# Kernel tuning notes

Measured on AMD Instinct MI355X. Metric: run time of the kernel, lower is better.

Reference implementation:

```python
import jax, jax.numpy as jnp
import numpy as np

B, NQ, NKV, D = 2, 2048, 4096, 1024
H, DH = 16, 64            # qk_channels = v_channels = 1024 -> 16 heads x 64
HID = 2 * int(4.0 * D)    # GEGLU produces 8192 -> split into 2x4096
EPS = 1e-6


def layernorm(x, scale, bias):
    mu = jnp.mean(x, axis=-1, keepdims=True)
    var = jnp.mean(jnp.square(x - mu), axis=-1, keepdims=True)
    return (x - mu) * jax.lax.rsqrt(var + EPS) * scale + bias


def setup_inputs() -> dict:
    key = jax.random.key(0)
    ks = jax.random.split(key, 12)
    s = 0.02
    return {
        "inputs_q": jax.random.normal(ks[0], (B, NQ, D), jnp.float32),
        "inputs_kv": jax.random.normal(ks[1], (B, NKV, D), jnp.float32),
        "ln_q_scale": jnp.ones((D,), jnp.float32),
        "ln_q_bias": jnp.zeros((D,), jnp.float32),
        "ln_kv_scale": jnp.ones((D,), jnp.float32),
        "ln_kv_bias": jnp.zeros((D,), jnp.float32),
        "Wq": s * jax.random.normal(ks[2], (D, H, DH), jnp.float32),
        "bq": jnp.zeros((H, DH), jnp.float32),
        "Wk": s * jax.random.normal(ks[3], (D, H, DH), jnp.float32),
        "bk": jnp.zeros((H, DH), jnp.float32),
        "Wv": s * jax.random.normal(ks[4], (D, H, DH), jnp.float32),
        "bv": jnp.zeros((H, DH), jnp.float32),
        "Wo": s * jax.random.normal(ks[5], (H, DH, D), jnp.float32),
        "bo": jnp.zeros((D,), jnp.float32),
        "ln2_scale": jnp.ones((D,), jnp.float32),
        "ln2_bias": jnp.zeros((D,), jnp.float32),
        "W1": s * jax.random.normal(ks[6], (D, HID), jnp.float32),
        "b1": jnp.zeros((HID,), jnp.float32),
        "W2": s * jax.random.normal(ks[7], (HID // 2, D), jnp.float32),
        "b2": jnp.zeros((D,), jnp.float32),
    }


def reference(inputs_q, inputs_kv, ln_q_scale, ln_q_bias, ln_kv_scale, ln_kv_bias,
              Wq, bq, Wk, bk, Wv, bv, Wo, bo, ln2_scale, ln2_bias, W1, b1, W2, b2):
    ln_q = layernorm(inputs_q, ln_q_scale, ln_q_bias)
    ln_kv = layernorm(inputs_kv, ln_kv_scale, ln_kv_bias)
    # multi-head projections: DenseGeneral to (H, DH)
    q = jnp.einsum('bqd,dhe->bqhe', ln_q, Wq) + bq
    k = jnp.einsum('bkd,dhe->bkhe', ln_kv, Wk) + bk
    v = jnp.einsum('bkd,dhe->bkhe', ln_kv, Wv) + bv
    # scaled dot-product attention (full score matrix, as in source)
    attn = jnp.einsum('bqhd,bkhd->bhqk', q, k) / np.sqrt(DH).astype(np.float32)
    attn = jax.nn.softmax(attn, axis=-1)
    o = jnp.einsum('bhqk,bkhd->bqhd', attn, v)
    # output projection contracting (H, DH)
    x = jnp.einsum('bqhd,hdo->bqo', o, Wo) + bo
    x = x + inputs_q  # query residual
    # GEGLU MLP
    h = layernorm(x, ln2_scale, ln2_bias)
    h = jnp.dot(h, W1) + b1
    a, g = jnp.split(h, 2, axis=-1)
    h = a * jax.nn.gelu(g)  # approximate (tanh) gelu, flax default
    y = jnp.dot(h, W2) + b2
    return x + y
```

## Files before the change

### kernel.cpp

```cpp
#include <hip/hip_runtime.h>

typedef unsigned short u16;
typedef unsigned int u32;
typedef float f32x4 __attribute__((ext_vector_type(4)));
typedef float f32x16 __attribute__((ext_vector_type(16)));
typedef __bf16 bf16x8 __attribute__((ext_vector_type(8)));
typedef short s16x8 __attribute__((ext_vector_type(8)));
typedef short s16x4 __attribute__((ext_vector_type(4)));
typedef u32 u32x4 __attribute__((ext_vector_type(4)));

#define MFMA16(a, b, c) __builtin_amdgcn_mfma_f32_16x16x32_bf16((a), (b), (c), 0, 0, 0)
#define MFMA32(a, b, c) __builtin_amdgcn_mfma_f32_32x32x16_bf16((a), (b), (c), 0, 0, 0)

typedef const __attribute__((address_space(1))) void* gas1_t;
typedef __attribute__((address_space(3))) void* las3_t;
#define GLDS16(g, l) __builtin_amdgcn_global_load_lds((gas1_t)(g), (las3_t)(l), 16, 0, 0)

static __device__ __forceinline__ u16 f2bf(float f) {
  u32 u = __builtin_bit_cast(u32, f);
  u += 0x7FFFu + ((u >> 16) & 1u);
  return (u16)(u >> 16);
}
static __device__ __forceinline__ u32 cvtpk(float lo, float hi) {
  u32 r;
  asm("v_cvt_pk_bf16_f32 %0, %1, %2" : "=v"(r) : "v"(lo), "v"(hi));
  return r;
}
static __device__ __forceinline__ float gelu_t(float g) {
  float u = 0.7978845608f * (g + 0.044715f * g * g * g);
  float e = __expf(2.0f * u);
  float t = 1.0f - 2.0f / (e + 1.0f);
  return 0.5f * g * (1.0f + t);
}

__global__ __launch_bounds__(256) void prep_weights(const float* __restrict__ Wq,
                                                    const float* __restrict__ Wk,
                                                    const float* __restrict__ Wv,
                                                    const float* __restrict__ Wo,
                                                    const float* __restrict__ W1,
                                                    const float* __restrict__ W2,
                                                    u16* __restrict__ wqt,
                                                    u16* __restrict__ wkvt,
                                                    u16* __restrict__ wot,
                                                    u16* __restrict__ w1i,
                                                    u16* __restrict__ w2t, float qsc) {
  __shared__ u16 t[64][72];
  const int id = blockIdx.x;
  const int tid = threadIdx.x;
  auto tileT = [&](const float* in, u16* out, int K, int N, int k0, int n0, float scale) {
#pragma unroll
    for (int i = 0; i < 16; ++i) {
      int idx = tid + i * 256;
      int r = idx >> 6, c = idx & 63;
      t[r][c] = f2bf(in[(size_t)(k0 + r) * N + n0 + c] * scale);
    }
    __syncthreads();
#pragma unroll
    for (int i = 0; i < 16; ++i) {
      int idx = tid + i * 256;
      int r = idx >> 6, c = idx & 63;
      out[(size_t)(n0 + r) * K + k0 + c] = t[c][r];
    }
  };
  if (id < 256) {
    tileT(Wq, wqt, 1024, 1024, (id & 15) * 64, (id >> 4) * 64, qsc);
  } else if (id < 512) {
    int i2 = id - 256;
    tileT(Wk, wkvt, 1024, 1024, (i2 & 15) * 64, (i2 >> 4) * 64, 1.0f);
  } else if (id < 768) {
    int i2 = id - 512;
    tileT(Wv, wkvt + 1024 * 1024, 1024, 1024, (i2 & 15) * 64, (i2 >> 4) * 64, 1.0f);
  } else if (id < 1024) {
    int i2 = id - 768;
    tileT(Wo, wot, 1024, 1024, (i2 & 15) * 64, (i2 >> 4) * 64, 1.0f);
  } else if (id < 3072) {
    int i2 = id - 1024;
    int k0 = (i2 & 15) * 64, n0 = (i2 >> 4) * 64;
#pragma unroll
    for (int i = 0; i < 16; ++i) {
      int idx = tid + i * 256;
      int r = idx >> 6, c = idx & 63;
      int np = n0 + c;
      int orig = ((np >> 5) << 4) + (np & 15) + (((np >> 4) & 1) << 12);
      t[r][c] = f2bf(W1[(size_t)(k0 + r) * 8192 + orig]);
    }
    __syncthreads();
#pragma unroll
    for (int i = 0; i < 16; ++i) {
      int idx = tid + i * 256;
      int r = idx >> 6, c = idx & 63;
      w1i[(size_t)(n0 + r) * 1024 + k0 + c] = t[c][r];
    }
  } else {
    int i3 = id - 3072;
    tileT(W2, w2t, 4096, 1024, (i3 & 63) * 64, (i3 >> 6) * 64, 1.0f);
  }
}

__global__ __launch_bounds__(256) void ln_fused(const float* __restrict__ xq,
                                                const float* __restrict__ xkv,
                                                const float* __restrict__ scq,
                                                const float* __restrict__ biq,
                                                const float* __restrict__ sckv,
                                                const float* __restrict__ bikv,
                                                u16* __restrict__ outq,
                                                u16* __restrict__ outkv) {
  const int id = blockIdx.x;
  const bool isq = id < 4096;
  const int row = isq ? id : id - 4096;
  const float* x = isq ? xq : xkv;
  const float* sc = isq ? scq : sckv;
  const float* bi = isq ? biq : bikv;
  u16* out = isq ? outq : outkv;
  int tid = threadIdx.x;
  float4 v = ((const float4*)(x + (size_t)row * 1024))[tid];
  float s = v.x + v.y + v.z + v.w;
  float s2 = v.x * v.x + v.y * v.y + v.z * v.z + v.w * v.w;
  for (int m = 1; m < 64; m <<= 1) {
    s += __shfl_xor(s, m);
    s2 += __shfl_xor(s2, m);
  }
  __shared__ float rs[4], rs2[4];
  int wave = tid >> 6, lane = tid & 63;
  if (lane == 0) { rs[wave] = s; rs2[wave] = s2; }
  __syncthreads();
  s = rs[0] + rs[1] + rs[2] + rs[3];
  s2 = rs2[0] + rs2[1] + rs2[2] + rs2[3];
  float mu = s * (1.0f / 1024.0f);
  float var = s2 * (1.0f / 1024.0f) - mu * mu;
  float inv = rsqrtf(var + 1e-6f);
  float4 scv = ((const float4*)sc)[tid];
  float4 biv = ((const float4*)bi)[tid];
  s16x4 o;
  o[0] = (short)f2bf((v.x - mu) * inv * scv.x + biv.x);
  o[1] = (short)f2bf((v.y - mu) * inv * scv.y + biv.y);
  o[2] = (short)f2bf((v.z - mu) * inv * scv.z + biv.z);
  o[3] = (short)f2bf((v.w - mu) * inv * scv.w + biv.w);
  *(s16x4*)(out + (size_t)row * 1024 + tid * 4) = o;
}

template <int MODE>
__global__ __launch_bounds__(256) void gemm_nt(const u16* __restrict__ A,
                                               const u16* __restrict__ Bt,
                                               const float* __restrict__ bias,
                                               const float* __restrict__ resid,
                                               void* __restrict__ Cout,
                                               int M, int N, int K, float bias_scale) {
  __shared__ u16 As[128 * 64];
  __shared__ u16 Bs[128 * 64];
  const int nbx = gridDim.x;
  const int nwg = nbx * gridDim.y;
  const int wg0 = blockIdx.y * nbx + blockIdx.x;
  const int wg = (nwg & 7) ? wg0 : (wg0 & 7) * (nwg >> 3) + (wg0 >> 3);
  const int m0 = (wg % nbx) * 128, n0 = (wg / nbx) * 128;
  const int tid = threadIdx.x;
  const int lane = tid & 63, wave = tid >> 6;
  const int wm = (wave >> 1) * 64, wn = (wave & 1) * 64;
  const int lr = lane & 15, hi4 = lane >> 4;
  f32x4 acc[4][4] = {};
  for (int k0 = 0; k0 < K; k0 += 64) {
#pragma unroll
    for (int i = 0; i < 4; ++i) {
      int s = i * 256 + tid;
      int r = s >> 3, slot = s & 7;
      int gslot = slot ^ (r & 7);
      int ldst = (i * 256 + wave * 64) * 8;
      GLDS16(A + (size_t)(m0 + r) * K + k0 + gslot * 8, &As[ldst]);
      GLDS16(Bt + (size_t)(n0 + r) * K + k0 + gslot * 8, &Bs[ldst]);
    }
    __syncthreads();
#pragma unroll
    for (int ks = 0; ks < 2; ++ks) {
      const int sl = ((ks * 4 + hi4) ^ (lr & 7)) * 8;
      bf16x8 af[4], bfr[4];
#pragma unroll
      for (int t = 0; t < 4; ++t) {
        af[t] = __builtin_bit_cast(bf16x8, *(const s16x8*)&As[(wm + t * 16 + lr) * 64 + sl]);
        bfr[t] = __builtin_bit_cast(bf16x8, *(const s16x8*)&Bs[(wn + t * 16 + lr) * 64 + sl]);
      }
#pragma unroll
      for (int mt = 0; mt < 4; ++mt)
#pragma unroll
        for (int nt = 0; nt < 4; ++nt)
          acc[mt][nt] = MFMA16(af[mt], bfr[nt], acc[mt][nt]);
    }
    __syncthreads();
  }
#pragma unroll
  for (int mt = 0; mt < 4; ++mt) {
#pragma unroll
    for (int nt = 0; nt < 4; ++nt) {
      const int ncol = n0 + wn + nt * 16 + lr;
      const float bv = bias[ncol] * bias_scale;
      const int mbase = m0 + wm + mt * 16 + hi4 * 4;
#pragma unroll
      for (int r = 0; r < 4; ++r) {
        const int m = mbase + r;
        const float val = acc[mt][nt][r] + bv;
        if constexpr (MODE == 0) {
          ((u16*)Cout)[(size_t)m * N + ncol] = f2bf(val);
        } else {
          ((float*)Cout)[(size_t)m * N + ncol] = val + resid[(size_t)m * N + ncol];
        }
      }
    }
  }
}

template <int MODE>
__global__ __launch_bounds__(512, 2) void gemm256(const u16* __restrict__ A,
                                                  const u16* __restrict__ Bt,
                                                  const float* __restrict__ bias,
                                                  const float* __restrict__ bias2,
                                                  u16* __restrict__ Cout,
                                                  u16* __restrict__ Vout,
                                                  int M, int N, int K, int nmajor) {
  __shared__ __align__(16) u16 sA[2][2][256 * 32];
  __shared__ __align__(16) u16 sB[2][2][256 * 32];
  const int nbx = M >> 8, nby = N >> 8;
  const int nblk = nbx * nby;
  const int cpx = nblk >> 3;
  const int wg0 = blockIdx.x;
  const int wg = (wg0 & 7) * cpx + (wg0 >> 3);
  int mi, ni;
  if (nmajor) { ni = wg % nby; mi = wg / nby; } else { mi = wg % nbx; ni = wg / nbx; }
  const int m0 = mi << 8, n0 = ni << 8;
  const int tid = threadIdx.x;
  const int lane = tid & 63, wave = tid >> 6;
  const int wr = wave >> 2, wc = wave & 3;
  const int lr = lane & 15, hi4 = lane >> 4;
  const int rdoct = (hi4 ^ ((lr >> 1) & 3)) * 8;
  const int NT = K >> 6;

  auto stageA = [&](int t, int kh) {
#pragma unroll
    for (int i = 0; i < 2; ++i) {
      int idx = i * 512 + tid;
      int r = idx >> 2, go = (idx & 3) ^ ((r >> 1) & 3);
      GLDS16(A + (size_t)(m0 + r) * K + t * 64 + kh * 32 + go * 8,
             &sA[t & 1][kh][(i * 512 + wave * 64) * 8]);
    }
  };
  auto stageB = [&](int t, int kh) {
#pragma unroll
    for (int i = 0; i < 2; ++i) {
      int idx = i * 512 + tid;
      int r = idx >> 2, go = (idx & 3) ^ ((r >> 1) & 3);
      GLDS16(Bt + (size_t)(n0 + r) * K + t * 64 + kh * 32 + go * 8,
             &sB[t & 1][kh][(i * 512 + wave * 64) * 8]);
    }
  };

  f32x4 acc[8][4] = {};
  bf16x8 af[4], bf[4];

  stageA(0, 0); stageB(0, 0); stageA(0, 1); stageB(0, 1);
  asm volatile("s_waitcnt vmcnt(4)" ::: "memory");
  __builtin_amdgcn_s_barrier();
  __builtin_amdgcn_sched_barrier(0);

  for (int t = 0; t < NT; ++t) {
    const int buf = t & 1;
    const bool pre = (t + 1 < NT);
#pragma unroll
    for (int kh = 0; kh < 2; ++kh) {
#pragma unroll
      for (int nt = 0; nt < 4; ++nt)
        bf[nt] = __builtin_bit_cast(bf16x8,
            *(const s16x8*)&sB[buf][kh][(wc * 64 + nt * 16 + lr) * 32 + rdoct]);
#pragma unroll
      for (int mf = 0; mf < 4; ++mf)
        af[mf] = __builtin_bit_cast(bf16x8,
            *(const s16x8*)&sA[buf][kh][(wr * 128 + mf * 16 + lr) * 32 + rdoct]);
      if (pre) stageA(t + 1, kh);
      __builtin_amdgcn_s_barrier();
      asm volatile("s_waitcnt lgkmcnt(0)" ::: "memory");
      __builtin_amdgcn_sched_barrier(0);
      __builtin_amdgcn_s_setprio(1);
#pragma unroll
      for (int mf = 0; mf < 4; ++mf)
#pragma unroll
        for (int nt = 0; nt < 4; ++nt)
          acc[mf][nt] = MFMA16(af[mf], bf[nt], acc[mf][nt]);
      __builtin_amdgcn_s_setprio(0);
      __builtin_amdgcn_s_barrier();
      __builtin_amdgcn_sched_barrier(0);
#pragma unroll
      for (int mf = 0; mf < 4; ++mf)
        af[mf] = __builtin_bit_cast(bf16x8,
            *(const s16x8*)&sA[buf][kh][(wr * 128 + (4 + mf) * 16 + lr) * 32 + rdoct]);
      if (pre) stageB(t + 1, kh);
      __builtin_amdgcn_s_barrier();
      asm volatile("s_waitcnt lgkmcnt(0)" ::: "memory");
      __builtin_amdgcn_sched_barrier(0);
      __builtin_amdgcn_s_setprio(1);
#pragma unroll
      for (int mf = 0; mf < 4; ++mf)
#pragma unroll
        for (int nt = 0; nt < 4; ++nt)
          acc[4 + mf][nt] = MFMA16(af[mf], bf[nt], acc[4 + mf][nt]);
      __builtin_amdgcn_s_setprio(0);
      if (pre)
        asm volatile("s_waitcnt vmcnt(4)" ::: "memory");
      else
        asm volatile("s_waitcnt vmcnt(0)" ::: "memory");
      __builtin_amdgcn_s_barrier();
      __builtin_amdgcn_sched_barrier(0);
    }
  }

  if constexpr (MODE == 0) {
#pragma unroll
    for (int mf = 0; mf < 8; ++mf) {
#pragma unroll
      for (int nt = 0; nt < 4; ++nt) {
        const int ncol = n0 + wc * 64 + nt * 16 + lr;
        const int mbase = m0 + wr * 128 + mf * 16 + hi4 * 4;
        const bool isk = ncol < 1024;
        const int vc = isk ? ncol : ncol - 1024;
        const float bv = isk ? bias[ncol] : bias2[vc];
#pragma unroll
        for (int r = 0; r < 4; ++r) {
          const int m = mbase + r;
          const float val = acc[mf][nt][r] + bv;
          if (isk) {
            Cout[(size_t)m * 1024 + ncol] = f2bf(val);
          } else {
            size_t vidx = ((size_t)((m >> 12) * 1024 + vc) << 12) | (size_t)(m & 4095);
            Vout[vidx] = f2bf(val);
          }
        }
      }
    }
  } else {
#pragma unroll
    for (int mf = 0; mf < 8; ++mf) {
      const int mbase = m0 + wr * 128 + mf * 16 + hi4 * 4;
#pragma unroll
      for (int p = 0; p < 2; ++p) {
        const int oc = (((n0 + wc * 64 + p * 32) >> 5) << 4) + lr;
        const float ba = bias[oc];
        const float bg = bias[oc + 4096];
#pragma unroll
        for (int r = 0; r < 4; ++r) {
          const int m = mbase + r;
          float a = acc[mf][2 * p][r] + ba;
          float g = acc[mf][2 * p + 1][r] + bg;
          Cout[(size_t)m * 4096 + oc] = f2bf(a * gelu_t(g));
        }
      }
    }
  }
}

__global__ __launch_bounds__(128, 3) void flash_attn(const u16* __restrict__ Qg,
                                                     const u16* __restrict__ Kg,
                                                     const u16* __restrict__ Vt,
                                                     u16* __restrict__ Og) {
  __shared__ u16 Ks[2][64 * 64];
  __shared__ u16 Vs[2][64 * 64];
  const int id = blockIdx.x;
  const int bh = (id & 7) * 4 + ((id >> 3) & 3);
  const int qb = id >> 5;
  const int b = bh >> 4, h = bh & 15;
  const int q0 = qb * 64;
  const int tid = threadIdx.x;
  const int lane = tid & 63, wave = tid >> 6;
  const int lq = lane & 31, hi = lane >> 5;
  const u16* Kbase = Kg + (size_t)(b * 4096) * 1024 + h * 64;
  const u16* Vbase = Vt + (size_t)((b * 16 + h) * 64) * 4096;
  bf16x8 qf[4];
  const size_t qrow = (size_t)(b * 2048 + q0 + wave * 32 + lq);
#pragma unroll
  for (int dc = 0; dc < 4; ++dc)
    qf[dc] = __builtin_bit_cast(bf16x8, *(const s16x8*)&Qg[qrow * 1024 + h * 64 + dc * 16 + hi * 8]);

  const u32x4 onesw = {0x3F803F80u, 0x3F803F80u, 0x3F803F80u, 0x3F803F80u};
  const bf16x8 ones = __builtin_bit_cast(bf16x8, onesw);
  f32x16 oacc0 = {}, oacc1 = {}, accl = {};

  auto stage = [&](int buf, int tile) {
    const int kv0 = tile * 64;
#pragma unroll
    for (int i = 0; i < 4; ++i) {
      int s = i * 128 + tid;
      int r = s >> 3;
      int inb = ((s & 7) * 16) ^ ((r & 7) << 4);
      GLDS16(Kbase + (size_t)(kv0 + r) * 1024 + (inb >> 1), &Ks[buf][s * 8]);
    }
#pragma unroll
    for (int i = 0; i < 4; ++i) {
      int s = i * 128 + tid;
      int r = s >> 3;
      int inb = ((s & 7) * 16) ^ ((r & 7) << 4);
      GLDS16(Vbase + (size_t)r * 4096 + kv0 + (inb >> 1), &Vs[buf][s * 8]);
    }
  };

  stage(0, 0);
  __syncthreads();
  int cur = 0;
  for (int t = 0; t < 64; ++t) {
    if (t < 63) stage(cur ^ 1, t + 1);
    f32x16 sA = {}, sB = {};
    __builtin_amdgcn_s_setprio(1);
#pragma unroll
    for (int dc = 0; dc < 4; ++dc) {
      int row = lq;
      int inb = (dc * 32 + hi * 16) ^ ((row & 7) << 4);
      bf16x8 kf = __builtin_bit_cast(bf16x8, *(const s16x8*)&Ks[cur][row * 64 + (inb >> 1)]);
      sA = MFMA32(kf, qf[dc], sA);
    }
#pragma unroll
    for (int dc = 0; dc < 4; ++dc) {
      int row = 32 + lq;
      int inb = (dc * 32 + hi * 16) ^ ((row & 7) << 4);
      bf16x8 kf = __builtin_bit_cast(bf16x8, *(const s16x8*)&Ks[cur][row * 64 + (inb >> 1)]);
      sB = MFMA32(kf, qf[dc], sB);
    }
    __builtin_amdgcn_s_setprio(0);
    bf16x8 vf0[4];
#pragma unroll
    for (int c = 0; c < 2; ++c) {
#pragma unroll
      for (int half = 0; half < 2; ++half) {
        int row = half * 32 + lq;
        int inb = (c * 32 + hi * 16) ^ ((row & 7) << 4);
        vf0[c * 2 + half] = __builtin_bit_cast(bf16x8, *(const s16x8*)&Vs[cur][row * 64 + (inb >> 1)]);
      }
    }
#pragma unroll
    for (int i = 0; i < 16; ++i) sA[i] = __builtin_amdgcn_exp2f(sA[i]);
#pragma unroll
    for (int i = 0; i < 16; ++i) sB[i] = __builtin_amdgcn_exp2f(sB[i]);
    u32 wa[8], wb[8];
#pragma unroll
    for (int i = 0; i < 8; ++i) wa[i] = cvtpk(sA[2 * i], sA[2 * i + 1]);
#pragma unroll
    for (int i = 0; i < 8; ++i) wb[i] = cvtpk(sB[2 * i], sB[2 * i + 1]);
    u32 a0 = wa[0], c0 = wa[2];
    asm("v_permlane32_swap_b32 %0, %1" : "+v"(a0), "+v"(c0));
    u32 a1 = wa[1], c1 = wa[3];
    asm("v_permlane32_swap_b32 %0, %1" : "+v"(a1), "+v"(c1));
    u32 a2 = wa[4], c2 = wa[6];
    asm("v_permlane32_swap_b32 %0, %1" : "+v"(a2), "+v"(c2));
    u32 a3 = wa[5], c3 = wa[7];
    asm("v_permlane32_swap_b32 %0, %1" : "+v"(a3), "+v"(c3));
    u32 e0 = wb[0], g0 = wb[2];
    asm("v_permlane32_swap_b32 %0, %1" : "+v"(e0), "+v"(g0));
    u32 e1 = wb[1], g1 = wb[3];
    asm("v_permlane32_swap_b32 %0, %1" : "+v"(e1), "+v"(g1));
    u32 e2 = wb[4], g2 = wb[6];
    asm("v_permlane32_swap_b32 %0, %1" : "+v"(e2), "+v"(g2));
    u32 e3 = wb[5], g3 = wb[7];
    asm("v_permlane32_swap_b32 %0, %1" : "+v"(e3), "+v"(g3));
    u32x4 t00 = {a0, a1, c0, c1};
    u32x4 t01 = {a2, a3, c2, c3};
    u32x4 t10 = {e0, e1, g0, g1};
    u32x4 t11 = {e2, e3, g2, g3};
    bf16x8 pf[4] = {__builtin_bit_cast(bf16x8, t00), __builtin_bit_cast(bf16x8, t01),
                    __builtin_bit_cast(bf16x8, t10), __builtin_bit_cast(bf16x8, t11)};
    __builtin_amdgcn_s_setprio(1);
#pragma unroll
    for (int c = 0; c < 2; ++c) {
      oacc0 = MFMA32(vf0[c * 2 + 0], pf[c], oacc0);
      oacc1 = MFMA32(vf0[c * 2 + 1], pf[c], oacc1);
      accl = MFMA32(ones, pf[c], accl);
    }
#pragma unroll
    for (int c = 0; c < 2; ++c) {
      {
        int row = lq;
        int inb = (64 + c * 32 + hi * 16) ^ ((row & 7) << 4);
        bf16x8 vf = __builtin_bit_cast(bf16x8, *(const s16x8*)&Vs[cur][row * 64 + (inb >> 1)]);
        oacc0 = MFMA32(vf, pf[2 + c], oacc0);
      }
      {
        int row = 32 + lq;
        int inb = (64 + c * 32 + hi * 16) ^ ((row & 7) << 4);
        bf16x8 vf = __builtin_bit_cast(bf16x8, *(const s16x8*)&Vs[cur][row * 64 + (inb >> 1)]);
        oacc1 = MFMA32(vf, pf[2 + c], oacc1);
      }
      accl = MFMA32(ones, pf[2 + c], accl);
    }
    __builtin_amdgcn_s_setprio(0);
    __syncthreads();
    cur ^= 1;
  }
  float rinv = 1.0f / accl[0];
  u16* obase = Og + qrow * 1024 + h * 64;
#pragma unroll
  for (int rp = 0; rp < 8; ++rp) {
    int r0 = rp * 2;
    int d0 = (r0 & 3) + 8 * (r0 >> 2) + 4 * hi;
    *(u32*)&obase[d0] = cvtpk(oacc0[r0] * rinv, oacc0[r0 + 1] * rinv);
    *(u32*)&obase[32 + d0] = cvtpk(oacc1[r0] * rinv, oacc1[r0 + 1] * rinv);
  }
}

extern "C" void kernel_launch(void* const* d_in, const int* in_sizes, int n_in,
                              void* d_out, int out_size, void* d_ws, size_t ws_size,
                              hipStream_t stream) {
  (void)in_sizes; (void)n_in; (void)out_size; (void)ws_size;
  const float* inputs_q = (const float*)d_in[0];
  const float* inputs_kv = (const float*)d_in[1];
  const float* ln_q_scale = (const float*)d_in[2];
  const float* ln_q_bias = (const float*)d_in[3];
  const float* ln_kv_scale = (const float*)d_in[4];
  const float* ln_kv_bias = (const float*)d_in[5];
  const float* Wq = (const float*)d_in[6];
  const float* bq = (const float*)d_in[7];
  const float* Wk = (const float*)d_in[8];
  const float* bk = (const float*)d_in[9];
  const float* Wv = (const float*)d_in[10];
  const float* bv = (const float*)d_in[11];
  const float* Wo = (const float*)d_in[12];
  const float* bo = (const float*)d_in[13];
  const float* ln2_scale = (const float*)d_in[14];
  const float* ln2_bias = (const float*)d_in[15];
  const float* W1 = (const float*)d_in[16];
  const float* b1 = (const float*)d_in[17];
  const float* W2 = (const float*)d_in[18];
  const float* b2 = (const float*)d_in[19];
  float* out = (float*)d_out;
  char* ws = (char*)d_ws;
  const size_t MB = 1ull << 20;
  u16* lnq = (u16*)(ws + 0);
  u16* lnkv = (u16*)(ws + 8 * MB);
  u16* Qb = (u16*)(ws + 24 * MB);
  u16* Kb = (u16*)(ws + 32 * MB);
  u16* Vtb = (u16*)(ws + 48 * MB);
  u16* Ob = (u16*)(ws + 64 * MB);
  float* xbuf = (float*)(ws + 72 * MB);
  u16* ln2b = (u16*)(ws + 88 * MB);
  u16* gg = (u16*)(ws + 96 * MB);
  u16* wqt = (u16*)(ws + 128 * MB);
  u16* wkvt = (u16*)(ws + 130 * MB);
  u16* wot = (u16*)(ws + 134 * MB);
  u16* w1i = (u16*)(ws + 136 * MB);
  u16* w2t = (u16*)(ws + 152 * MB);

  const float QSC = 0.125f * 1.44269504088896f;
  dim3 blk(256);
  prep_weights<<<dim3(4096), blk, 0, stream>>>(Wq, Wk, Wv, Wo, W1, W2, wqt, wkvt, wot, w1i, w2t, QSC);
  ln_fused<<<dim3(12288), blk, 0, stream>>>(inputs_q, inputs_kv, ln_q_scale, ln_q_bias,
                                            ln_kv_scale, ln_kv_bias, lnq, lnkv);
  gemm_nt<0><<<dim3(32, 8), blk, 0, stream>>>(lnq, wqt, bq, nullptr, Qb, 4096, 1024, 1024, QSC);
  gemm256<0><<<dim3(256), dim3(512), 0, stream>>>(lnkv, wkvt, bk, bv, Kb, Vtb, 8192, 2048, 1024, 1);
  flash_attn<<<dim3(1024), dim3(128), 0, stream>>>(Qb, Kb, Vtb, Ob);
  gemm_nt<2><<<dim3(32, 8), blk, 0, stream>>>(Ob, wot, bo, inputs_q, xbuf, 4096, 1024, 1024, 1.0f);
  ln_fused<<<dim3(4096), blk, 0, stream>>>(xbuf, xbuf, ln2_scale, ln2_bias, ln2_scale, ln2_bias,
                                           ln2b, ln2b);
  gemm256<1><<<dim3(512), dim3(512), 0, stream>>>(ln2b, w1i, b1, nullptr, gg, nullptr, 4096, 8192, 1024, 0);
  gemm_nt<2><<<dim3(32, 8), blk, 0, stream>>>(gg, w2t, b2, xbuf, out, 4096, 1024, 4096, 1.0f);
}
```

Measured before the change: 408.0 us.

## Restructure flash attention: 256-row query tiles, triple-buffered KV, VALU row sums

```diff
diff --git a/kernel.cpp b/kernel.cpp
--- a/kernel.cpp
+++ b/kernel.cpp
@@ -353,148 +353,171 @@
   }
 }
 
-__global__ __launch_bounds__(128, 3) void flash_attn(const u16* __restrict__ Qg,
+__global__ __launch_bounds__(256, 1) void flash_attn(const u16* __restrict__ Qg,
                                                      const u16* __restrict__ Kg,
                                                      const u16* __restrict__ Vt,
                                                      u16* __restrict__ Og) {
-  __shared__ u16 Ks[2][64 * 64];
-  __shared__ u16 Vs[2][64 * 64];
+  __shared__ u16 Ks[3][64 * 64];
+  __shared__ u16 Vs[3][64 * 64];
   const int id = blockIdx.x;
-  const int bh = (id & 7) * 4 + ((id >> 3) & 3);
+  const int rr = id & 31;
+  const int bh = (rr & 7) * 4 + (rr >> 3);
   const int qb = id >> 5;
   const int b = bh >> 4, h = bh & 15;
-  const int q0 = qb * 64;
+  const int q0 = qb * 256;
   const int tid = threadIdx.x;
   const int lane = tid & 63, wave = tid >> 6;
   const int lq = lane & 31, hi = lane >> 5;
   const u16* Kbase = Kg + (size_t)(b * 4096) * 1024 + h * 64;
   const u16* Vbase = Vt + (size_t)((b * 16 + h) * 64) * 4096;
-  bf16x8 qf[4];
-  const size_t qrow = (size_t)(b * 2048 + q0 + wave * 32 + lq);
-#pragma unroll
-  for (int dc = 0; dc < 4; ++dc)
-    qf[dc] = __builtin_bit_cast(bf16x8, *(const s16x8*)&Qg[qrow * 1024 + h * 64 + dc * 16 + hi * 8]);
-
-  const u32x4 onesw = {0x3F803F80u, 0x3F803F80u, 0x3F803F80u, 0x3F803F80u};
-  const bf16x8 ones = __builtin_bit_cast(bf16x8, onesw);
-  f32x16 oacc0 = {}, oacc1 = {}, accl = {};
+  bf16x8 qf0[4], qf1[4];
+  const size_t qrow0 = (size_t)(b * 2048 + q0 + wave * 64 + lq);
+  const size_t qrow1 = qrow0 + 32;
+#pragma unroll
+  for (int dc = 0; dc < 4; ++dc) {
+    qf0[dc] = __builtin_bit_cast(bf16x8, *(const s16x8*)&Qg[qrow0 * 1024 + h * 64 + dc * 16 + hi * 8]);
+    qf1[dc] = __builtin_bit_cast(bf16x8, *(const s16x8*)&Qg[qrow1 * 1024 + h * 64 + dc * 16 + hi * 8]);
+  }
+  f32x16 oacc00 = {}, oacc01 = {}, oacc10 = {}, oacc11 = {};
+  float l0 = 0.0f, l1 = 0.0f;
 
   auto stage = [&](int buf, int tile) {
     const int kv0 = tile * 64;
 #pragma unroll
-    for (int i = 0; i < 4; ++i) {
-      int s = i * 128 + tid;
+    for (int i = 0; i < 2; ++i) {
+      int s = i * 256 + tid;
       int r = s >> 3;
       int inb = ((s & 7) * 16) ^ ((r & 7) << 4);
-      GLDS16(Kbase + (size_t)(kv0 + r) * 1024 + (inb >> 1), &Ks[buf][s * 8]);
-    }
-#pragma unroll
-    for (int i = 0; i < 4; ++i) {
-      int s = i * 128 + tid;
+      GLDS16(Kbase + (size_t)(kv0 + r) * 1024 + (inb >> 1), &Ks[buf][(i * 256 + wave * 64) * 8]);
+    }
+#pragma unroll
+    for (int i = 0; i < 2; ++i) {
+      int s = i * 256 + tid;
       int r = s >> 3;
       int inb = ((s & 7) * 16) ^ ((r & 7) << 4);
-      GLDS16(Vbase + (size_t)r * 4096 + kv0 + (inb >> 1), &Vs[buf][s * 8]);
+      GLDS16(Vbase + (size_t)r * 4096 + kv0 + (inb >> 1), &Vs[buf][(i * 256 + wave * 64) * 8]);
     }
   };
 
+  auto softpack = [&](f32x16 sA, f32x16 sB, bf16x8* pf, float& lrun) {
+#pragma unroll
+    for (int i = 0; i < 16; ++i) sA[i] = __builtin_amdgcn_exp2f(sA[i]);
+#pragma unroll
+    for (int i = 0; i < 16; ++i) sB[i] = __builtin_amdgcn_exp2f(sB[i]);
+    float a0 = (sA[0] + sA[1]) + (sA[2] + sA[3]);
+    float a1 = (sA[4] + sA[5]) + (sA[6] + sA[7]);
+    float a2 = (sA[8] + sA[9]) + (sA[10] + sA[11]);
+    float a3 = (sA[12] + sA[13]) + (sA[14] + sA[15]);
+    float b0 = (sB[0] + sB[1]) + (sB[2] + sB[3]);
+    float b1 = (sB[4] + sB[5]) + (sB[6] + sB[7]);
+    float b2 = (sB[8] + sB[9]) + (sB[10] + sB[11]);
+    float b3 = (sB[12] + sB[13]) + (sB[14] + sB[15]);
+    float ts = ((a0 + a1) + (a2 + a3)) + ((b0 + b1) + (b2 + b3));
+    ts += __shfl_xor(ts, 32);
+    lrun += ts;
+    u32 wa[8], wb[8];
+#pragma unroll
+    for (int i = 0; i < 8; ++i) wa[i] = cvtpk(sA[2 * i], sA[2 * i + 1]);
+#pragma unroll
+    for (int i = 0; i < 8; ++i) wb[i] = cvtpk(sB[2 * i], sB[2 * i + 1]);
+    u32 x0 = wa[0], y0 = wa[2];
+    asm("v_permlane32_swap_b32 %0, %1" : "+v"(x0), "+v"(y0));
+    u32 x1 = wa[1], y1 = wa[3];
+    asm("v_permlane32_swap_b32 %0, %1" : "+v"(x1), "+v"(y1));
+    u32 x2 = wa[4], y2 = wa[6];
+    asm("v_permlane32_swap_b32 %0, %1" : "+v"(x2), "+v"(y2));
+    u32 x3 = wa[5], y3 = wa[7];
+    asm("v_permlane32_swap_b32 %0, %1" : "+v"(x3), "+v"(y3));
+    u32 z0 = wb[0], u0 = wb[2];
+    asm("v_permlane32_swap_b32 %0, %1" : "+v"(z0), "+v"(u0));
+    u32 z1 = wb[1], u1 = wb[3];
+    asm("v_permlane32_swap_b32 %0, %1" : "+v"(z1), "+v"(u1));
+    u32 z2 = wb[4], u2 = wb[6];
+    asm("v_permlane32_swap_b32 %0, %1" : "+v"(z2), "+v"(u2));
+    u32 z3 = wb[5], u3 = wb[7];
+    asm("v_permlane32_swap_b32 %0, %1" : "+v"(z3), "+v"(u3));
+    u32x4 t00 = {x0, x1, y0, y1};
+    u32x4 t01 = {x2, x3, y2, y3};
+    u32x4 t10 = {z0, z1, u0, u1};
+    u32x4 t11 = {z2, z3, u2, u3};
+    pf[0] = __builtin_bit_cast(bf16x8, t00);
+    pf[1] = __builtin_bit_cast(bf16x8, t01);
+    pf[2] = __builtin_bit_cast(bf16x8, t10);
+    pf[3] = __builtin_bit_cast(bf16x8, t11);
+  };
+
   stage(0, 0);
-  __syncthreads();
-  int cur = 0;
+  stage(1, 1);
+  asm volatile("s_waitcnt vmcnt(4)" ::: "memory");
+  __builtin_amdgcn_s_barrier();
+  __builtin_amdgcn_sched_barrier(0);
+
   for (int t = 0; t < 64; ++t) {
-    if (t < 63) stage(cur ^ 1, t + 1);
+    const int buf = t % 3;
+    if (t + 2 < 64) stage((t + 2) % 3, t + 2);
+    bf16x8 kf[8];
+#pragma unroll
+    for (int st = 0; st < 2; ++st)
+#pragma unroll
+      for (int dc = 0; dc < 4; ++dc) {
+        int row = st * 32 + lq;
+        int inb = (dc * 32 + hi * 16) ^ ((row & 7) << 4);
+        kf[st * 4 + dc] = __builtin_bit_cast(bf16x8, *(const s16x8*)&Ks[buf][row * 64 + (inb >> 1)]);
+      }
     f32x16 sA = {}, sB = {};
     __builtin_amdgcn_s_setprio(1);
 #pragma unroll
-    for (int dc = 0; dc < 4; ++dc) {
-      int row = lq;
-      int inb = (dc * 32 + hi * 16) ^ ((row & 7) << 4);
-      bf16x8 kf = __builtin_bit_cast(bf16x8, *(const s16x8*)&Ks[cur][row * 64 + (inb >> 1)]);
-      sA = MFMA32(kf, qf[dc], sA);
-    }
-#pragma unroll
-    for (int dc = 0; dc < 4; ++dc) {
-      int row = 32 + lq;
-      int inb = (dc * 32 + hi * 16) ^ ((row & 7) << 4);
-      bf16x8 kf = __builtin_bit_cast(bf16x8, *(const s16x8*)&Ks[cur][row * 64 + (inb >> 1)]);
-      sB = MFMA32(kf, qf[dc], sB);
-    }
+    for (int dc = 0; dc < 4; ++dc) sA = MFMA32(kf[dc], qf0[dc], sA);
+#pragma unroll
+    for (int dc = 0; dc < 4; ++dc) sB = MFMA32(kf[4 + dc], qf0[dc], sB);
     __builtin_amdgcn_s_setprio(0);
-    bf16x8 vf0[4];
-#pragma unroll
-    for (int c = 0; c < 2; ++c) {
-#pragma unroll
-      for (int half = 0; half < 2; ++half) {
-        int row = half * 32 + lq;
-        int inb = (c * 32 + hi * 16) ^ ((row & 7) << 4);
-        vf0[c * 2 + half] = __builtin_bit_cast(bf16x8, *(const s16x8*)&Vs[cur][row * 64 + (inb >> 1)]);
+    bf16x8 pf0[4];
+    softpack(sA, sB, pf0, l0);
+    f32x16 tA = {}, tB = {};
+    __builtin_amdgcn_s_setprio(1);
+#pragma unroll
+    for (int dc = 0; dc < 4; ++dc) tA = MFMA32(kf[dc], qf1[dc], tA);
+#pragma unroll
+    for (int dc = 0; dc < 4; ++dc) tB = MFMA32(kf[4 + dc], qf1[dc], tB);
+    __builtin_amdgcn_s_setprio(0);
+    bf16x8 pf1[4];
+    softpack(tA, tB, pf1, l1);
+    __builtin_amdgcn_s_setprio(1);
+#pragma unroll
+    for (int st = 0; st < 2; ++st)
+#pragma unroll
+      for (int c = 0; c < 2; ++c) {
+        const int pi = st * 2 + c;
+        int rowa = lq;
+        int inba = (st * 64 + c * 32 + hi * 16) ^ ((rowa & 7) << 4);
+        bf16x8 vfa = __builtin_bit_cast(bf16x8, *(const s16x8*)&Vs[buf][rowa * 64 + (inba >> 1)]);
+        int rowb = 32 + lq;
+        int inbb = (st * 64 + c * 32 + hi * 16) ^ ((rowb & 7) << 4);
+        bf16x8 vfb = __builtin_bit_cast(bf16x8, *(const s16x8*)&Vs[buf][rowb * 64 + (inbb >> 1)]);
+        oacc00 = MFMA32(vfa, pf0[pi], oacc00);
+        oacc01 = MFMA32(vfb, pf0[pi], oacc01);
+        oacc10 = MFMA32(vfa, pf1[pi], oacc10);
+        oacc11 = MFMA32(vfb, pf1[pi], oacc11);
       }
-    }
-#pragma unroll
-    for (int i = 0; i < 16; ++i) sA[i] = __builtin_amdgcn_exp2f(sA[i]);
-#pragma unroll
-    for (int i = 0; i < 16; ++i) sB[i] = __builtin_amdgcn_exp2f(sB[i]);
-    u32 wa[8], wb[8];
-#pragma unroll
-    for (int i = 0; i < 8; ++i) wa[i] = cvtpk(sA[2 * i], sA[2 * i + 1]);
-#pragma unroll
-    for (int i = 0; i < 8; ++i) wb[i] = cvtpk(sB[2 * i], sB[2 * i + 1]);
-    u32 a0 = wa[0], c0 = wa[2];
-    asm("v_permlane32_swap_b32 %0, %1" : "+v"(a0), "+v"(c0));
-    u32 a1 = wa[1], c1 = wa[3];
-    asm("v_permlane32_swap_b32 %0, %1" : "+v"(a1), "+v"(c1));
-    u32 a2 = wa[4], c2 = wa[6];
-    asm("v_permlane32_swap_b32 %0, %1" : "+v"(a2), "+v"(c2));
-    u32 a3 = wa[5], c3 = wa[7];
-    asm("v_permlane32_swap_b32 %0, %1" : "+v"(a3), "+v"(c3));
-    u32 e0 = wb[0], g0 = wb[2];
-    asm("v_permlane32_swap_b32 %0, %1" : "+v"(e0), "+v"(g0));
-    u32 e1 = wb[1], g1 = wb[3];
-    asm("v_permlane32_swap_b32 %0, %1" : "+v"(e1), "+v"(g1));
-    u32 e2 = wb[4], g2 = wb[6];
-    asm("v_permlane32_swap_b32 %0, %1" : "+v"(e2), "+v"(g2));
-    u32 e3 = wb[5], g3 = wb[7];
-    asm("v_permlane32_swap_b32 %0, %1" : "+v"(e3), "+v"(g3));
-    u32x4 t00 = {a0, a1, c0, c1};
-    u32x4 t01 = {a2, a3, c2, c3};
-    u32x4 t10 = {e0, e1, g0, g1};
-    u32x4 t11 = {e2, e3, g2, g3};
-    bf16x8 pf[4] = {__builtin_bit_cast(bf16x8, t00), __builtin_bit_cast(bf16x8, t01),
-                    __builtin_bit_cast(bf16x8, t10), __builtin_bit_cast(bf16x8, t11)};
-    __builtin_amdgcn_s_setprio(1);
-#pragma unroll
-    for (int c = 0; c < 2; ++c) {
-      oacc0 = MFMA32(vf0[c * 2 + 0], pf[c], oacc0);
-      oacc1 = MFMA32(vf0[c * 2 + 1], pf[c], oacc1);
-      accl = MFMA32(ones, pf[c], accl);
-    }
-#pragma unroll
-    for (int c = 0; c < 2; ++c) {
-      {
-        int row = lq;
-        int inb = (64 + c * 32 + hi * 16) ^ ((row & 7) << 4);
-        bf16x8 vf = __builtin_bit_cast(bf16x8, *(const s16x8*)&Vs[cur][row * 64 + (inb >> 1)]);
-        oacc0 = MFMA32(vf, pf[2 + c], oacc0);
-      }
-      {
-        int row = 32 + lq;
-        int inb = (64 + c * 32 + hi * 16) ^ ((row & 7) << 4);
-        bf16x8 vf = __builtin_bit_cast(bf16x8, *(const s16x8*)&Vs[cur][row * 64 + (inb >> 1)]);
-        oacc1 = MFMA32(vf, pf[2 + c], oacc1);
-      }
-      accl = MFMA32(ones, pf[2 + c], accl);
-    }
     __builtin_amdgcn_s_setprio(0);
-    __syncthreads();
-    cur ^= 1;
-  }
-  float rinv = 1.0f / accl[0];
-  u16* obase = Og + qrow * 1024 + h * 64;
+    if (t + 2 < 64)
+      asm volatile("s_waitcnt vmcnt(4)" ::: "memory");
+    else
+      asm volatile("s_waitcnt vmcnt(0)" ::: "memory");
+    __builtin_amdgcn_s_barrier();
+    __builtin_amdgcn_sched_barrier(0);
+  }
+  const float r0v = 1.0f / l0, r1v = 1.0f / l1;
+  u16* ob0 = Og + qrow0 * 1024 + h * 64;
+  u16* ob1 = Og + qrow1 * 1024 + h * 64;
 #pragma unroll
   for (int rp = 0; rp < 8; ++rp) {
     int r0 = rp * 2;
     int d0 = (r0 & 3) + 8 * (r0 >> 2) + 4 * hi;
-    *(u32*)&obase[d0] = cvtpk(oacc0[r0] * rinv, oacc0[r0 + 1] * rinv);
-    *(u32*)&obase[32 + d0] = cvtpk(oacc1[r0] * rinv, oacc1[r0 + 1] * rinv);
+    *(u32*)&ob0[d0] = cvtpk(oacc00[r0] * r0v, oacc00[r0 + 1] * r0v);
+    *(u32*)&ob0[32 + d0] = cvtpk(oacc01[r0] * r0v, oacc01[r0 + 1] * r0v);
+    *(u32*)&ob1[d0] = cvtpk(oacc10[r0] * r1v, oacc10[r0 + 1] * r1v);
+    *(u32*)&ob1[32 + d0] = cvtpk(oacc11[r0] * r1v, oacc11[r0 + 1] * r1v);
   }
 }
 
@@ -547,7 +570,7 @@
                                             ln_kv_scale, ln_kv_bias, lnq, lnkv);
   gemm_nt<0><<<dim3(32, 8), blk, 0, stream>>>(lnq, wqt, bq, nullptr, Qb, 4096, 1024, 1024, QSC);
   gemm256<0><<<dim3(256), dim3(512), 0, stream>>>(lnkv, wkvt, bk, bv, Kb, Vtb, 8192, 2048, 1024, 1);
-  flash_attn<<<dim3(1024), dim3(128), 0, stream>>>(Qb, Kb, Vtb, Ob);
+  flash_attn<<<dim3(256), blk, 0, stream>>>(Qb, Kb, Vtb, Ob);
   gemm_nt<2><<<dim3(32, 8), blk, 0, stream>>>(Ob, wot, bo, inputs_q, xbuf, 4096, 1024, 1024, 1.0f);
   ln_fused<<<dim3(4096), blk, 0, stream>>>(xbuf, xbuf, ln2_scale, ln2_bias, ln2_scale, ln2_bias,
                                            ln2b, ln2b);
```

After: 419.1 us. 2.7% more time.
